# Performance work log

Hardware: AMD Instinct MI355X
Metric: run time of the kernel (lower is better)

The kernel has to match this reference:

```python
import jax, jax.numpy as jnp
import numpy as np

B, L, D_MODEL = 2, 1024, 1024
H, HD, W = 16, 64, 64  # heads, head_dim, window_size


def setup_inputs() -> dict:
    key = jax.random.key(0)
    ks = jax.random.split(key, 5)
    s = 1.0 / np.sqrt(D_MODEL).astype(np.float32)
    x = jax.random.normal(ks[0], (B, L, D_MODEL), jnp.float32)
    Wq = jax.random.normal(ks[1], (D_MODEL, D_MODEL), jnp.float32) * s
    Wk = jax.random.normal(ks[2], (D_MODEL, D_MODEL), jnp.float32) * s
    Wv = jax.random.normal(ks[3], (D_MODEL, D_MODEL), jnp.float32) * s
    Wo = jax.random.normal(ks[4], (D_MODEL, D_MODEL), jnp.float32) * s
    # RoPE angles: theta[l, j] = l / 10000^(2j/HD), shape (1, L, HD//2)
    pos = jnp.arange(L, dtype=jnp.float32)
    inv_freq = 1.0 / (10000.0 ** (jnp.arange(0, HD, 2, dtype=jnp.float32) / HD))
    freqs = (pos[:, None] * inv_freq[None, :])[None]  # (1, L, HD//2)
    return {"x": x, "freqs": freqs, "Wq": Wq, "Wk": Wk, "Wv": Wv, "Wo": Wo}


def reference(x, freqs, Wq, Wk, Wv, Wo):
    b, l, _ = x.shape
    # projections -> (B, H, L, HD)
    def heads(t):
        return t.reshape(b, l, H, HD).transpose(0, 2, 1, 3)
    q, k, v = heads(x @ Wq), heads(x @ Wk), heads(x @ Wv)

    # RoPE (complex multiply on interleaved pairs, matching view_as_complex)
    cos = jnp.cos(freqs)[:, None]  # (1, 1, L, HD//2)
    sin = jnp.sin(freqs)[:, None]
    def rope(t):
        t2 = t.reshape(b, H, l, HD // 2, 2)
        re, im = t2[..., 0], t2[..., 1]
        return jnp.stack([re * cos - im * sin, re * sin + im * cos], axis=-1).reshape(b, H, l, HD)
    q, k = rope(q), rope(k)

    # causal sliding windows: pad W-1 zeros on the left, gather windows
    pad = W - 1
    kp = jnp.pad(k, ((0, 0), (0, 0), (pad, 0), (0, 0)))
    vp = jnp.pad(v, ((0, 0), (0, 0), (pad, 0), (0, 0)))
    idx = jnp.arange(l)[:, None] + jnp.arange(W)[None, :]  # (L, W)
    kw = kp[:, :, idx]  # (B, H, L, W, HD)
    vw = vp[:, :, idx]

    scores = jnp.einsum('bhld,bhlwd->bhlw', q, kw) / np.sqrt(HD).astype(np.float32)
    attn = jax.nn.softmax(scores, axis=-1)
    out = jnp.einsum('bhlw,bhlwd->bhld', attn, vw)
    out = out.transpose(0, 2, 1, 3).reshape(b, l, D_MODEL)
    return out @ Wo
```

## Files before the change

kernel.cpp:

```cpp
#include <hip/hip_runtime.h>

#define LSEQ 1024
#define NBATCH 2
#define NH 16
#define HDIM 64
#define WWIN 64
#define M_GEMM 2048
#define K_GEMM 1024
#define N_GEMM 1024
#define PLANE_ELEMS (1u << 21)

#define BKT 64

typedef __bf16 bf16x8 __attribute__((ext_vector_type(8)));
typedef _Float16 f16x8 __attribute__((ext_vector_type(8)));
typedef float f32x4 __attribute__((ext_vector_type(4)));

typedef __attribute__((address_space(1))) const unsigned int gas_uint;
typedef __attribute__((address_space(3))) unsigned int las_uint;

__device__ __forceinline__ unsigned short f2bf(float f) {
  unsigned int u = __float_as_uint(f);
  u += 0x7fff + ((u >> 16) & 1);
  return (unsigned short)(u >> 16);
}
__device__ __forceinline__ unsigned short f2h(float f) {
  const _Float16 h = (_Float16)f;
  return __builtin_bit_cast(unsigned short, h);
}

union F16_8 { f16x8 v; unsigned short u[8]; };

__global__ void prep_all_k(const float* __restrict__ x,
                           unsigned short* __restrict__ xb,
                           const float* __restrict__ freqs,
                           float* __restrict__ ctab, float* __restrict__ stab,
                           const float* __restrict__ W0,
                           const float* __restrict__ W1,
                           const float* __restrict__ W2,
                           const float* __restrict__ W3,
                           unsigned short* __restrict__ Wt,
                           unsigned short* __restrict__ zp) {
  __shared__ float tile[32][33];
  const int bid = blockIdx.x;
  const int tid = threadIdx.x;
  if (bid < 2048) {
    const int i = bid * 256 + tid;
    const float4 v = reinterpret_cast<const float4*>(x)[i];
    ushort4 o;
    o.x = f2bf(v.x); o.y = f2bf(v.y); o.z = f2bf(v.z); o.w = f2bf(v.w);
    reinterpret_cast<ushort4*>(xb)[i] = o;
  } else if (bid < 2176) {
    const int i = (bid - 2048) * 256 + tid;
    float s, c;
    sincosf(freqs[i], &s, &c);
    ctab[i] = c;
    stab[i] = s;
  } else if (bid < 6272) {
    const int t = bid - 2176;
    const int z = t >> 10;
    const float* src = (z == 0) ? W0 : (z == 1) ? W1 : (z == 2) ? W2 : W3;
    unsigned short* dst = Wt + ((size_t)z << 20);
    const int rem = t & 1023;
    const int n0 = (rem & 31) << 5, k0 = (rem >> 5) << 5;
    const int tx = tid & 31, ty = tid >> 5;
#pragma unroll
    for (int i = 0; i < 32; i += 8)
      tile[ty + i][tx] = src[(size_t)(k0 + ty + i) * 1024 + n0 + tx];
    __syncthreads();
#pragma unroll
    for (int i = 0; i < 32; i += 8)
      dst[(size_t)(n0 + ty + i) * 1024 + k0 + tx] = f2bf(tile[tx][ty + i]);
  } else {
    ushort4 zz = {0, 0, 0, 0};
    reinterpret_cast<ushort4*>(zp)[tid] = zz;
  }
}

__device__ __forceinline__ void gload16(const void* g, void* l) {
  __builtin_amdgcn_global_load_lds((gas_uint*)g, (las_uint*)l, 16, 0, 0);
}

template <int MODE, int TBM, int TBN, int WN, int THREADS>
__global__ __launch_bounds__(THREADS, (THREADS == 512) ? 6 : 4) void gemm_bf16_k(
    const unsigned short* __restrict__ A,
    const unsigned short* __restrict__ Bt0,
    void* __restrict__ C0,
    const float* __restrict__ ctab,
    const float* __restrict__ stab) {
  constexpr int NBM = M_GEMM / TBM;
  constexpr int NBN = N_GEMM / TBN;
  constexpr int NZ = (MODE == 0) ? 3 : 1;
  constexpr int CW = TBN / WN;
  constexpr int NJ = CW / 16;
  constexpr int MI = TBM / 16;
  constexpr int ASZ = TBM * BKT;
  constexpr int BSZ = TBN * BKT;
  constexpr int RND = THREADS * 8;
  constexpr int ASL = ASZ / RND;
  constexpr int BSL = BSZ / RND;
  constexpr int NT = K_GEMM / BKT;
  constexpr int CPX = NBM * NBN * NZ / 8;
  __shared__ unsigned short sA[2 * ASZ];
  __shared__ unsigned short sB[2 * BSZ];

  const int tid = threadIdx.x;
  const int lane = tid & 63;
  const int wave = tid >> 6;
  const int wn = wave;

  const int p = blockIdx.x;
  const int lid = (p & 7) * CPX + (p >> 3);
  const int z = lid / (NBM * NBN);
  const int rem = lid % (NBM * NBN);
  const int bm = rem % NBM;
  const int bn = rem / NBM;

  const unsigned short* Bt = Bt0 + (size_t)z * ((size_t)N_GEMM * K_GEMM);
  const int m0 = bm * TBM, n0 = bn * TBN;

  const int skoff = (((tid & 7) ^ ((tid >> 3) & 7)) << 3);

  const unsigned short* gA[ASL];
  const unsigned short* gB[BSL];
#pragma unroll
  for (int s = 0; s < ASL; ++s)
    gA[s] = A + (size_t)(m0 + s * (THREADS / 8) + (tid >> 3)) * K_GEMM + skoff;
#pragma unroll
  for (int s = 0; s < BSL; ++s)
    gB[s] = Bt + (size_t)(n0 + s * (THREADS / 8) + (tid >> 3)) * K_GEMM + skoff;

  f32x4 acc[MI][NJ] = {};

  const int fr = lane & 15;
  const int lg = lane >> 4;
  const int co0 = ((lg ^ (fr & 7)) << 3);
  const int co1 = co0 ^ 32;

#pragma unroll
  for (int s = 0; s < ASL; ++s) gload16(gA[s], sA + (s * THREADS + tid) * 8);
#pragma unroll
  for (int s = 0; s < BSL; ++s) gload16(gB[s], sB + (s * THREADS + tid) * 8);
  __syncthreads();

#pragma unroll 2
  for (int t = 0; t < NT; ++t) {
    const int cur = t & 1;
    const int nxt = cur ^ 1;
    if (t + 1 < NT) {
      const int kt = (t + 1) * BKT;
#pragma unroll
      for (int s = 0; s < ASL; ++s)
        gload16(gA[s] + kt, sA + nxt * ASZ + (s * THREADS + tid) * 8);
#pragma unroll
      for (int s = 0; s < BSL; ++s)
        gload16(gB[s] + kt, sB + nxt * BSZ + (s * THREADS + tid) * 8);
    }
    const unsigned short* cA = sA + cur * ASZ;
    const unsigned short* cB = sB + cur * BSZ;
    bf16x8 af[2][MI], bfr[2][NJ];
#pragma unroll
    for (int i = 0; i < MI; i++) {
      af[0][i] = *reinterpret_cast<const bf16x8*>(&cA[(i * 16 + fr) * BKT + co0]);
      af[1][i] = *reinterpret_cast<const bf16x8*>(&cA[(i * 16 + fr) * BKT + co1]);
    }
#pragma unroll
    for (int j = 0; j < NJ; j++) {
      bfr[0][j] = *reinterpret_cast<const bf16x8*>(&cB[(wn * CW + j * 16 + fr) * BKT + co0]);
      bfr[1][j] = *reinterpret_cast<const bf16x8*>(&cB[(wn * CW + j * 16 + fr) * BKT + co1]);
    }
#pragma unroll
    for (int ks = 0; ks < 2; ks++)
#pragma unroll
      for (int i = 0; i < MI; i++)
#pragma unroll
        for (int j = 0; j < NJ; j++)
          acc[i][j] = __builtin_amdgcn_mfma_f32_16x16x32_bf16(af[ks][i], bfr[ks][j], acc[i][j], 0, 0, 0);
    __syncthreads();
  }

  const int fq = lane >> 4;
  const bool dorope = (MODE == 0) && (z < 2);
#pragma unroll
  for (int i = 0; i < MI; i++) {
#pragma unroll
    for (int j = 0; j < NJ; j++) {
#pragma unroll
      for (int r = 0; r < 4; r++) {
        const int row = m0 + i * 16 + fq * 4 + r;
        const int col = n0 + wn * CW + j * 16 + fr;
        float v = acc[i][j][r];
        if (MODE == 0) {
          const int l = row & 1023, d = col & 63;
          if (dorope) {
            const float other = __shfl_xor(v, 1);
            const int ti = (l << 5) + (d >> 1);
            const float c = ctab[ti], s = stab[ti];
            v = (d & 1) ? (other * s + v * c) : (v * c - other * s);
          }
          if (z == 0) v *= 0.125f;
          const float vp = __shfl_xor(v, 1);
          if (!(fr & 1)) {
            const int b = row >> 10, h = col >> 6;
            const size_t idx = ((((size_t)b * NH + h) * LSEQ + l) << 6) + d;
            const unsigned int pk = (unsigned)f2h(v) | ((unsigned)f2h(vp) << 16);
            ((unsigned int*)C0)[((size_t)z * PLANE_ELEMS + idx) >> 1] = pk;
          }
        } else {
          ((float*)C0)[(size_t)row * N_GEMM + col] = v;
        }
      }
    }
  }
}

__device__ __forceinline__ int kaddr(int j, int d) {
  return j * 128 + ((((d >> 3) ^ (j & 7)) & 7) << 4) + ((d & 7) << 1);
}
__device__ __forceinline__ int taddr(int r, int c) {
  return r * 256 + ((((c >> 3) ^ (r & 7)) & 15) << 4) + ((c & 7) << 1);
}

__global__ __launch_bounds__(256, 2) void local_attn5_k(
    const unsigned short* __restrict__ planes,
    const unsigned short* __restrict__ zp,
    unsigned short* __restrict__ O) {
  __shared__ __align__(16) unsigned char KsF[16384];
  __shared__ __align__(16) unsigned char VtB[16384];
  __shared__ __align__(16) unsigned char PsB[16384];

  const int tid = threadIdx.x;
  const int lane = tid & 63;
  const int wave = tid >> 6;
  const int lr = lane & 15;
  const int lg = lane >> 4;
  const int pb = blockIdx.x;
  const int lid = (pb & 7) * 64 + (pb >> 3);
  const int bh = lid >> 4;
  const int lb = (lid & 15) << 6;

  const unsigned short* QFb = planes + ((size_t)bh << 16);
  const unsigned short* KFb = planes + (size_t)PLANE_ELEMS + ((size_t)bh << 16);
  const unsigned short* VFb = planes + 2 * (size_t)PLANE_ELEMS + ((size_t)bh << 16);

#pragma unroll
  for (int r = 0; r < 4; ++r) {
    const int item = r * 256 + tid;
    const int j = item >> 3;
    const int c = item & 7;
    const int g = lb - 64 + j;
    const int sc = ((c ^ (j & 7)) << 3);
    const unsigned short* sK = (g >= 0) ? KFb + ((size_t)g << 6) + sc : zp + (c << 3);
    gload16(sK, KsF + item * 16);
  }

#pragma unroll
  for (int pp = 0; pp < 4; ++pp) {
    const int item = pp * 256 + tid;
    const int jp = item >> 4;
    const int d0 = (item & 15) << 2;
    const int g0 = lb - 64 + 2 * jp;
    ushort4 a = {0, 0, 0, 0}, b = {0, 0, 0, 0};
    if (g0 >= 0) a = *reinterpret_cast<const ushort4*>(VFb + ((size_t)g0 << 6) + d0);
    if (g0 + 1 >= 0) b = *reinterpret_cast<const ushort4*>(VFb + ((size_t)(g0 + 1) << 6) + d0);
    *reinterpret_cast<unsigned int*>(VtB + taddr(d0 + 0, 2 * jp)) = (unsigned)a.x | ((unsigned)b.x << 16);
    *reinterpret_cast<unsigned int*>(VtB + taddr(d0 + 1, 2 * jp)) = (unsigned)a.y | ((unsigned)b.y << 16);
    *reinterpret_cast<unsigned int*>(VtB + taddr(d0 + 2, 2 * jp)) = (unsigned)a.z | ((unsigned)b.z << 16);
    *reinterpret_cast<unsigned int*>(VtB + taddr(d0 + 3, 2 * jp)) = (unsigned)a.w | ((unsigned)b.w << 16);
  }
  __syncthreads();

  const int rtbase = wave * 16;
  const size_t qoff = ((size_t)(lb + rtbase + lr) << 6);
  F16_8 qf[2];
#pragma unroll
  for (int ks = 0; ks < 2; ++ks)
    qf[ks].v = *reinterpret_cast<const f16x8*>(QFb + qoff + ks * 32 + lg * 8);

  f32x4 acc[8] = {};
#pragma unroll
  for (int ks = 0; ks < 2; ++ks) {
    const int d0 = ks * 32 + lg * 8;
#pragma unroll
    for (int nt = 0; nt < 8; ++nt) {
      const int j = nt * 16 + lr;
      const f16x8 kf = *reinterpret_cast<const f16x8*>(KsF + kaddr(j, d0));
      acc[nt] = __builtin_amdgcn_mfma_f32_16x16x32_f16(qf[ks].v, kf, acc[nt], 0, 0, 0);
    }
  }

  float sum4[4];
#pragma unroll
  for (int reg = 0; reg < 4; ++reg) {
    const int rt = rtbase + lg * 4 + reg;
    float m = -3.0e38f;
#pragma unroll
    for (int nt = 0; nt < 8; ++nt) {
      const int j = nt * 16 + lr;
      const bool valid = (j > rt) && (j <= rt + 64);
      const float sv = valid ? acc[nt][reg] : -3.0e38f;
      acc[nt][reg] = sv;
      m = fmaxf(m, sv);
    }
    m = fmaxf(m, __shfl_xor(m, 1));
    m = fmaxf(m, __shfl_xor(m, 2));
    m = fmaxf(m, __shfl_xor(m, 4));
    m = fmaxf(m, __shfl_xor(m, 8));
    float s = 0.f;
#pragma unroll
    for (int nt = 0; nt < 8; ++nt) {
      const float pv = (acc[nt][reg] > -1.0e37f) ? __expf(acc[nt][reg] - m) : 0.f;
      acc[nt][reg] = pv;
      s += pv;
    }
    s += __shfl_xor(s, 1);
    s += __shfl_xor(s, 2);
    s += __shfl_xor(s, 4);
    s += __shfl_xor(s, 8);
    sum4[reg] = s;
  }

#pragma unroll
  for (int nt = 0; nt < 8; ++nt)
#pragma unroll
    for (int reg = 0; reg < 4; ++reg) {
      const int rt = rtbase + lg * 4 + reg;
      const int j = nt * 16 + lr;
      *reinterpret_cast<unsigned short*>(PsB + taddr(rt, j)) = f2h(acc[nt][reg]);
    }

  f32x4 oacc[4] = {};
#pragma unroll
  for (int ks = 0; ks < 4; ++ks) {
    const int j0 = ks * 32 + lg * 8;
    const f16x8 pa = *reinterpret_cast<const f16x8*>(PsB + taddr(rtbase + lr, j0));
#pragma unroll
    for (int nt = 0; nt < 4; ++nt) {
      const int d = nt * 16 + lr;
      const f16x8 vf = *reinterpret_cast<const f16x8*>(VtB + taddr(d, j0));
      oacc[nt] = __builtin_amdgcn_mfma_f32_16x16x32_f16(pa, vf, oacc[nt], 0, 0, 0);
    }
  }

  const int b = bh >> 4, h = bh & 15;
#pragma unroll
  for (int nt = 0; nt < 4; ++nt)
#pragma unroll
    for (int reg = 0; reg < 4; ++reg) {
      const int rt = rtbase + lg * 4 + reg;
      const int d = nt * 16 + lr;
      const float o = oacc[nt][reg] / sum4[reg];
      const int lq = lb + rt;
      O[(((size_t)b * LSEQ + lq) << 10) + (h << 6) + d] = f2bf(o);
    }
}

extern "C" void kernel_launch(void* const* d_in, const int* in_sizes, int n_in,
                              void* d_out, int out_size, void* d_ws, size_t ws_size,
                              hipStream_t stream) {
  const float* x     = (const float*)d_in[0];
  const float* freqs = (const float*)d_in[1];
  const float* Wq    = (const float*)d_in[2];
  const float* Wk    = (const float*)d_in[3];
  const float* Wv    = (const float*)d_in[4];
  const float* Wo    = (const float*)d_in[5];
  float* out = (float*)d_out;
  char* ws = (char*)d_ws;

  unsigned short* xb     = (unsigned short*)ws;
  unsigned short* Wt     = (unsigned short*)(ws + (4u << 20));
  unsigned short* planes = (unsigned short*)(ws + (12u << 20));
  unsigned short* Oat    = (unsigned short*)(ws + (24u << 20));
  float* ctab = (float*)(ws + (28u << 20));
  float* stab = ctab + 32768;
  unsigned short* zp = (unsigned short*)(ws + (28u << 20) + (1u << 19));

  prep_all_k<<<6273, 256, 0, stream>>>(x, xb, freqs, ctab, stab, Wq, Wk, Wv, Wo, Wt, zp);

  gemm_bf16_k<0, 64, 128, 8, 512><<<768, 512, 0, stream>>>(xb, Wt, planes, ctab, stab);

  local_attn5_k<<<512, 256, 0, stream>>>(planes, zp, Oat);

  gemm_bf16_k<1, 32, 64, 4, 256><<<1024, 256, 0, stream>>>(Oat, Wt + (3u << 20), out, ctab, stab);
}
```

Baseline: 54.25 us.

## Use 32x32x16 MFMA with 2x4 wave grid in QKV projection GEMM

Result: slower. 55.96 us (+3.2%).

```diff
diff --git a/kernel.cpp b/kernel.cpp
--- a/kernel.cpp
+++ b/kernel.cpp
@@ -15,6 +15,7 @@
 typedef __bf16 bf16x8 __attribute__((ext_vector_type(8)));
 typedef _Float16 f16x8 __attribute__((ext_vector_type(8)));
 typedef float f32x4 __attribute__((ext_vector_type(4)));
+typedef float f32x16 __attribute__((ext_vector_type(16)));
 
 typedef __attribute__((address_space(1))) const unsigned int gas_uint;
 typedef __attribute__((address_space(3))) unsigned int las_uint;
@@ -81,16 +82,117 @@
   __builtin_amdgcn_global_load_lds((gas_uint*)g, (las_uint*)l, 16, 0, 0);
 }
 
-template <int MODE, int TBM, int TBN, int WN, int THREADS>
-__global__ __launch_bounds__(THREADS, (THREADS == 512) ? 6 : 4) void gemm_bf16_k(
+__global__ __launch_bounds__(512, 6) void gemm_qkv32_k(
     const unsigned short* __restrict__ A,
     const unsigned short* __restrict__ Bt0,
-    void* __restrict__ C0,
+    unsigned short* __restrict__ C0,
     const float* __restrict__ ctab,
     const float* __restrict__ stab) {
+  constexpr int TBM = 64, TBN = 128;
   constexpr int NBM = M_GEMM / TBM;
   constexpr int NBN = N_GEMM / TBN;
-  constexpr int NZ = (MODE == 0) ? 3 : 1;
+  constexpr int ASZ = TBM * BKT;
+  constexpr int BSZ = TBN * BKT;
+  constexpr int NT = K_GEMM / BKT;
+  constexpr int CPX = NBM * NBN * 3 / 8;
+  __shared__ unsigned short sA[2 * ASZ];
+  __shared__ unsigned short sB[2 * BSZ];
+
+  const int tid = threadIdx.x;
+  const int lane = tid & 63;
+  const int wave = tid >> 6;
+  const int wm = wave >> 2;
+  const int wn = wave & 3;
+  const int l31 = lane & 31;
+  const int hi = lane >> 5;
+  const int lo7 = lane & 7;
+
+  const int p = blockIdx.x;
+  const int lid = (p & 7) * CPX + (p >> 3);
+  const int z = lid / (NBM * NBN);
+  const int rem = lid % (NBM * NBN);
+  const int bm = rem % NBM;
+  const int bn = rem / NBM;
+
+  const unsigned short* Bt = Bt0 + (size_t)z * ((size_t)N_GEMM * K_GEMM);
+  const int m0 = bm * TBM, n0 = bn * TBN;
+
+  const int skoff = (((tid & 7) ^ ((tid >> 3) & 7)) << 3);
+
+  const unsigned short* gA0 = A + (size_t)(m0 + (tid >> 3)) * K_GEMM + skoff;
+  const unsigned short* gB0 = Bt + (size_t)(n0 + (tid >> 3)) * K_GEMM + skoff;
+  const unsigned short* gB1 = Bt + (size_t)(n0 + 64 + (tid >> 3)) * K_GEMM + skoff;
+
+  f32x16 acc = {};
+
+  int co[4];
+#pragma unroll
+  for (int ks = 0; ks < 4; ++ks) co[ks] = (((ks * 2 + hi) ^ lo7) << 3);
+  const int arow = (wm * 32 + l31) * BKT;
+  const int brow = (wn * 32 + l31) * BKT;
+
+  gload16(gA0, sA + tid * 8);
+  gload16(gB0, sB + tid * 8);
+  gload16(gB1, sB + (512 + tid) * 8);
+  __syncthreads();
+
+#pragma unroll 2
+  for (int t = 0; t < NT; ++t) {
+    const int cur = t & 1;
+    const int nxt = cur ^ 1;
+    if (t + 1 < NT) {
+      const int kt = (t + 1) * BKT;
+      gload16(gA0 + kt, sA + nxt * ASZ + tid * 8);
+      gload16(gB0 + kt, sB + nxt * BSZ + tid * 8);
+      gload16(gB1 + kt, sB + nxt * BSZ + (512 + tid) * 8);
+    }
+    const unsigned short* cA = sA + cur * ASZ;
+    const unsigned short* cB = sB + cur * BSZ;
+    bf16x8 af[4], bfr[4];
+#pragma unroll
+    for (int ks = 0; ks < 4; ++ks) {
+      af[ks] = *reinterpret_cast<const bf16x8*>(&cA[arow + co[ks]]);
+      bfr[ks] = *reinterpret_cast<const bf16x8*>(&cB[brow + co[ks]]);
+    }
+#pragma unroll
+    for (int ks = 0; ks < 4; ++ks)
+      acc = __builtin_amdgcn_mfma_f32_32x32x16_bf16(af[ks], bfr[ks], acc, 0, 0, 0);
+    __syncthreads();
+  }
+
+  const bool dorope = (z < 2);
+  const int colg = n0 + wn * 32 + l31;
+  const int d = colg & 63;
+  const int h = colg >> 6;
+#pragma unroll
+  for (int reg = 0; reg < 16; ++reg) {
+    const int row = m0 + wm * 32 + (reg & 3) + 8 * (reg >> 2) + 4 * hi;
+    const int l = row & 1023;
+    float v = acc[reg];
+    if (dorope) {
+      const float other = __shfl_xor(v, 1);
+      const int ti = (l << 5) + (d >> 1);
+      const float c = ctab[ti], s = stab[ti];
+      v = (d & 1) ? (other * s + v * c) : (v * c - other * s);
+    }
+    if (z == 0) v *= 0.125f;
+    const float vp = __shfl_xor(v, 1);
+    if (!(lane & 1)) {
+      const int b = row >> 10;
+      const size_t idx = ((((size_t)b * NH + h) * LSEQ + l) << 6) + d;
+      const unsigned int pk = (unsigned)f2h(v) | ((unsigned)f2h(vp) << 16);
+      reinterpret_cast<unsigned int*>(C0)[((size_t)z * PLANE_ELEMS + idx) >> 1] = pk;
+    }
+  }
+}
+
+template <int TBM, int TBN, int WN, int THREADS>
+__global__ __launch_bounds__(THREADS, 4) void gemm_out_k(
+    const unsigned short* __restrict__ A,
+    const unsigned short* __restrict__ Bt,
+    float* __restrict__ C0) {
+  constexpr int NBM = M_GEMM / TBM;
+  constexpr int NBN = N_GEMM / TBN;
   constexpr int CW = TBN / WN;
   constexpr int NJ = CW / 16;
   constexpr int MI = TBM / 16;
@@ -100,7 +202,7 @@
   constexpr int ASL = ASZ / RND;
   constexpr int BSL = BSZ / RND;
   constexpr int NT = K_GEMM / BKT;
-  constexpr int CPX = NBM * NBN * NZ / 8;
+  constexpr int CPX = NBM * NBN / 8;
   __shared__ unsigned short sA[2 * ASZ];
   __shared__ unsigned short sB[2 * BSZ];
 
@@ -111,14 +213,10 @@
 
   const int p = blockIdx.x;
   const int lid = (p & 7) * CPX + (p >> 3);
-  const int z = lid / (NBM * NBN);
-  const int rem = lid % (NBM * NBN);
-  const int bm = rem % NBM;
-  const int bn = rem / NBM;
-
-  const unsigned short* Bt = Bt0 + (size_t)z * ((size_t)N_GEMM * K_GEMM);
+  const int bm = lid % NBM;
+  const int bn = lid / NBM;
+
   const int m0 = bm * TBM, n0 = bn * TBN;
-
   const int skoff = (((tid & 7) ^ ((tid >> 3) & 7)) << 3);
 
   const unsigned short* gA[ASL];
@@ -180,38 +278,16 @@
   }
 
   const int fq = lane >> 4;
-  const bool dorope = (MODE == 0) && (z < 2);
-#pragma unroll
-  for (int i = 0; i < MI; i++) {
-#pragma unroll
-    for (int j = 0; j < NJ; j++) {
+#pragma unroll
+  for (int i = 0; i < MI; i++)
+#pragma unroll
+    for (int j = 0; j < NJ; j++)
 #pragma unroll
       for (int r = 0; r < 4; r++) {
         const int row = m0 + i * 16 + fq * 4 + r;
         const int col = n0 + wn * CW + j * 16 + fr;
-        float v = acc[i][j][r];
-        if (MODE == 0) {
-          const int l = row & 1023, d = col & 63;
-          if (dorope) {
-            const float other = __shfl_xor(v, 1);
-            const int ti = (l << 5) + (d >> 1);
-            const float c = ctab[ti], s = stab[ti];
-            v = (d & 1) ? (other * s + v * c) : (v * c - other * s);
-          }
-          if (z == 0) v *= 0.125f;
-          const float vp = __shfl_xor(v, 1);
-          if (!(fr & 1)) {
-            const int b = row >> 10, h = col >> 6;
-            const size_t idx = ((((size_t)b * NH + h) * LSEQ + l) << 6) + d;
-            const unsigned int pk = (unsigned)f2h(v) | ((unsigned)f2h(vp) << 16);
-            ((unsigned int*)C0)[((size_t)z * PLANE_ELEMS + idx) >> 1] = pk;
-          }
-        } else {
-          ((float*)C0)[(size_t)row * N_GEMM + col] = v;
-        }
+        C0[(size_t)row * N_GEMM + col] = acc[i][j][r];
       }
-    }
-  }
 }
 
 __device__ __forceinline__ int kaddr(int j, int d) {
@@ -377,9 +453,9 @@
 
   prep_all_k<<<6273, 256, 0, stream>>>(x, xb, freqs, ctab, stab, Wq, Wk, Wv, Wo, Wt, zp);
 
-  gemm_bf16_k<0, 64, 128, 8, 512><<<768, 512, 0, stream>>>(xb, Wt, planes, ctab, stab);
+  gemm_qkv32_k<<<768, 512, 0, stream>>>(xb, Wt, planes, ctab, stab);
 
   local_attn5_k<<<512, 256, 0, stream>>>(planes, zp, Oat);
 
-  gemm_bf16_k<1, 32, 64, 4, 256><<<1024, 256, 0, stream>>>(Oat, Wt + (3u << 20), out, ctab, stab);
-}
+  gemm_out_k<32, 64, 4, 256><<<1024, 256, 0, stream>>>(Oat, Wt + (3u << 20), out);
+}
```
